# Kernel tuning notes

Hardware: AMD Instinct MI355X
Metric: run time of the kernel (lower is better)

## Reference

```python
import jax, jax.numpy as jnp
import numpy as np

WINDOW = 128
LOOK_BACKWARD = 1
LOOK_FORWARD = 0
DIM_HEAD = 64
ROPE_BASE = 10000.0


def look_around(x, backward=LOOK_BACKWARD, forward=LOOK_FORWARD, pad_value=-1):
    # x: [b, w, n, ...] -> pad window axis, gather shifted windows, concat along n axis
    w = x.shape[1]
    pads = [(0, 0)] * x.ndim
    pads[1] = (backward, forward)
    padded = jnp.pad(x, pads, constant_values=pad_value)
    return jnp.concatenate([padded[:, i:i + w] for i in range(backward + forward + 1)], axis=2)


def _rotate_half(x):
    x1, x2 = jnp.split(x, 2, axis=-1)
    return jnp.concatenate([-x2, x1], axis=-1)


def apply_rotary(bq, bk):
    # sinusoidal embeddings computed over the look-around key length j; queries use the last n positions
    j = bk.shape[2]
    n = bq.shape[2]
    inv_freq = 1.0 / (ROPE_BASE ** (jnp.arange(0, DIM_HEAD, 2, dtype=jnp.float32) / DIM_HEAD))
    t = jnp.arange(j, dtype=jnp.float32)
    freqs = t[:, None] * inv_freq[None, :]          # [j, d/2]
    freqs = jnp.concatenate([freqs, freqs], axis=-1)  # [j, d]
    q_freqs = freqs[-n:]
    bq = bq * jnp.cos(q_freqs) + _rotate_half(bq) * jnp.sin(q_freqs)
    bk = bk * jnp.cos(freqs) + _rotate_half(bk) * jnp.sin(freqs)
    return bq, bk


def setup_inputs() -> dict:
    key = jax.random.key(0)
    kq, kk, kv = jax.random.split(key, 3)
    shape = (4, 8, 4096, 64)
    return {
        'q': jax.random.normal(kq, shape, dtype=jnp.float32),
        'k': jax.random.normal(kk, shape, dtype=jnp.float32),
        'v': jax.random.normal(kv, shape, dtype=jnp.float32),
    }


def reference(q, k, v):
    B, H, N, D = q.shape
    b = B * H
    q_ = q.reshape(b, N, D)
    k_ = k.reshape(b, N, D)
    v_ = v.reshape(b, N, D)
    w = N // WINDOW
    scale = D ** -0.5

    seq = jnp.arange(N)
    b_t = seq.reshape(1, w, WINDOW)                           # [1, w, n]

    bq = q_.reshape(b, w, WINDOW, D) * scale
    bk = look_around(k_.reshape(b, w, WINDOW, D), pad_value=-1.0)  # [b, w, j, d]
    bv = look_around(v_.reshape(b, w, WINDOW, D), pad_value=-1.0)

    bq, bk = apply_rotary(bq, bk)

    bq_t = b_t[..., :, None]                                  # [1, w, n, 1]
    bq_k = look_around(b_t, pad_value=-1)[..., None, :]        # [1, w, 1, j]
    pad_mask = bq_k == -1
    causal_mask = bq_t < bq_k

    sim = jnp.einsum('bwie,bwje->bwij', bq, bk)                # [b, w, n, j]
    mask_value = -jnp.finfo(sim.dtype).max
    sim = jnp.where(causal_mask | pad_mask, mask_value, sim)

    attn = jax.nn.softmax(sim, axis=-1)
    out = jnp.einsum('bwij,bwje->bwie', attn, bv)
    return out.reshape(B, H, N, D)
```

## Files before the change

kernel.cpp:

```cpp
#include <hip/hip_runtime.h>
#include <float.h>

typedef __attribute__((ext_vector_type(8))) _Float16 f16x8;
typedef __attribute__((ext_vector_type(4))) _Float16 f16x4;
typedef __attribute__((ext_vector_type(4))) float f32x4;

#define WIN 128
#define SEQ 4096
#define DH 64
#define KSTR 72
#define VSTR 260
#define PC 40
#define VOFF 36864
#define POFF (VOFF + DH * VSTR * 2)
#define L2B_OVER 0.41524101186092156f

__launch_bounds__(512, 4)
__global__ void lattn_kernel(const float* __restrict__ q,
                             const float* __restrict__ k,
                             const float* __restrict__ v,
                             float* __restrict__ out) {
  __shared__ __align__(16) char smem[POFF + 8 * 16 * PC * 2];
  _Float16* ksm = (_Float16*)smem;
  _Float16* vsm = (_Float16*)(smem + VOFF);
  _Float16* psm = (_Float16*)(smem + POFF);

  const int bid  = blockIdx.x;
  const int lbid = (bid & 7) * 128 + (bid >> 3);
  const int bh   = lbid >> 5;
  const int win  = lbid & 31;
  const int tid  = threadIdx.x;
  const int wv   = tid >> 6;
  const int lane = tid & 63;
  const int c    = lane & 15;
  const int g    = lane >> 4;

  const long kbase = (long)win * WIN - WIN;
  const float* kb = k + (size_t)bh * SEQ * DH;
  const float* vb = v + (size_t)bh * SEQ * DH;


  float4 klo[4], khi[4];
  #pragma unroll
  for (int it = 0; it < 4; ++it) {
    int hi  = it * 8 + wv;
    int row = c + 16 * (hi >> 1);
    int p   = g + 4 * (hi & 1);
    long grow = kbase + row; grow = grow < 0 ? 0 : grow;
    const float4* src = (const float4*)(kb + grow * DH);
    klo[it] = src[p];
    khi[it] = src[p + 8];
  }

  float4 vr[2][4];
  #pragma unroll
  for (int it = 0; it < 2; ++it) {
    int kq = g + 4 * (it * 8 + wv);
    #pragma unroll
    for (int i = 0; i < 4; ++i) {
      long grow = kbase + 4 * kq + i; grow = grow < 0 ? 0 : grow;
      vr[it][i] = *(const float4*)(vb + grow * DH + 4 * c);
    }
  }

  const int qrow = 16 * wv + c;
  const float* qp = q + ((size_t)bh * SEQ + (size_t)win * WIN + qrow) * DH;
  const float4 x0 = *(const float4*)(qp + 8 * g);
  const float4 x1 = *(const float4*)(qp + 8 * g + 4);
  const float4 y0 = *(const float4*)(qp + 8 * g + 32);
  const float4 y1 = *(const float4*)(qp + 8 * g + 36);

  #pragma unroll
  for (int it = 0; it < 4; ++it) {
    int hi  = it * 8 + wv;
    int row = c + 16 * (hi >> 1);
    int p   = g + 4 * (hi & 1);
    float pos = (float)row;
    f16x4 rl, rh;
    #pragma unroll
    for (int j = 0; j < 4; ++j) {
      float sn, cs;
      __sincosf(pos * exp2f(-(float)(4 * p + j) * L2B_OVER), &sn, &cs);
      float x = ((const float*)&klo[it])[j];
      float y = ((const float*)&khi[it])[j];
      rl[j] = (_Float16)(x * cs - y * sn);
      rh[j] = (_Float16)(y * cs + x * sn);
    }
    *(f16x4*)(&ksm[row * KSTR + 4 * p])      = rl;
    *(f16x4*)(&ksm[row * KSTR + 4 * p + 32]) = rh;
  }

  #pragma unroll
  for (int it = 0; it < 2; ++it) {
    int kq = g + 4 * (it * 8 + wv);
    #pragma unroll
    for (int j = 0; j < 4; ++j) {
      f16x4 w;
      #pragma unroll
      for (int i = 0; i < 4; ++i) w[i] = (_Float16)(((const float*)&vr[it][i])[j]);
      *(f16x4*)(&vsm[(4 * c + j) * VSTR + 4 * kq]) = w;
    }
  }

  f16x8 qf0, qf1;
  {
    float pos = (float)(128 + qrow);
    #pragma unroll
    for (int j = 0; j < 4; ++j) {
      float sn, cs;
      __sincosf(pos * exp2f(-(float)(8 * g + j) * L2B_OVER), &sn, &cs);
      float xa = ((const float*)&x0)[j], ya = ((const float*)&y0)[j];
      qf0[j]     = (_Float16)((xa * cs - ya * sn) * 0.125f);
      qf1[j]     = (_Float16)((ya * cs + xa * sn) * 0.125f);
      __sincosf(pos * exp2f(-(float)(8 * g + 4 + j) * L2B_OVER), &sn, &cs);
      float xb = ((const float*)&x1)[j], yb = ((const float*)&y1)[j];
      qf0[4 + j] = (_Float16)((xb * cs - yb * sn) * 0.125f);
      qf1[4 + j] = (_Float16)((yb * cs + xb * sn) * 0.125f);
    }
  }

  __syncthreads();

  f32x4 acc[16];
  #pragma unroll
  for (int mt = 0; mt < 16; ++mt) acc[mt] = (f32x4){0.f, 0.f, 0.f, 0.f};

  #pragma unroll
  for (int mt = 0; mt < 16; ++mt) {
    f16x8 kf0 = *(const f16x8*)(&ksm[(16 * mt + c) * KSTR + 8 * g]);
    f16x8 kf1 = *(const f16x8*)(&ksm[(16 * mt + c) * KSTR + 32 + 8 * g]);
    acc[mt] = __builtin_amdgcn_mfma_f32_16x16x32_f16(kf0, qf0, acc[mt], 0, 0, 0);
    acc[mt] = __builtin_amdgcn_mfma_f32_16x16x32_f16(kf1, qf1, acc[mt], 0, 0, 0);
  }

  const int qi   = qrow;
  const int kmin = (win == 0) ? 128 : 0;
  float m = -FLT_MAX;
  #pragma unroll
  for (int mt = 0; mt < 16; ++mt) {
    #pragma unroll
    for (int r = 0; r < 4; ++r) {
      int j = 16 * mt + 4 * g + r;
      bool ok = (j <= qi + 128) && (j >= kmin);
      float s = ok ? acc[mt][r] : -FLT_MAX;
      acc[mt][r] = s;
      m = fmaxf(m, s);
    }
  }
  m = fmaxf(m, __shfl_xor(m, 16));
  m = fmaxf(m, __shfl_xor(m, 32));

  float sm = 0.f;
  #pragma unroll
  for (int mt = 0; mt < 16; ++mt) {
    #pragma unroll
    for (int r = 0; r < 4; ++r) {
      float p = __expf(acc[mt][r] - m);
      acc[mt][r] = p;
      sm += p;
    }
  }
  sm += __shfl_xor(sm, 16);
  sm += __shfl_xor(sm, 32);
  const float rinv = 1.0f / sm;

  f32x4 oacc[4];
  #pragma unroll
  for (int nt = 0; nt < 4; ++nt) oacc[nt] = (f32x4){0.f, 0.f, 0.f, 0.f};

  _Float16* pw = psm + wv * 16 * PC;

  #pragma unroll
  for (int ks = 0; ks < 8; ++ks) {
    #pragma unroll
    for (int t = 0; t < 2; ++t) {
      int mt = 2 * ks + t;
      f16x4 pv4;
      #pragma unroll
      for (int r = 0; r < 4; ++r) pv4[r] = (_Float16)(acc[mt][r] * rinv);
      *(f16x4*)(&pw[c * PC + 16 * t + 4 * g]) = pv4;
    }
    f16x8 pf = *(const f16x8*)(&pw[c * PC + 8 * g]);
    #pragma unroll
    for (int nt = 0; nt < 4; ++nt) {
      f16x8 vf = *(const f16x8*)(&vsm[(16 * nt + c) * VSTR + 32 * ks + 8 * g]);
      oacc[nt] = __builtin_amdgcn_mfma_f32_16x16x32_f16(vf, pf, oacc[nt], 0, 0, 0);
    }
  }

  float* ob = out + ((size_t)bh * SEQ + (size_t)win * WIN + qrow) * DH;
  #pragma unroll
  for (int nt = 0; nt < 4; ++nt) {
    float4 o4 = {oacc[nt][0], oacc[nt][1], oacc[nt][2], oacc[nt][3]};
    *(float4*)(ob + 16 * nt + 4 * g) = o4;
  }
}

extern "C" void kernel_launch(void* const* d_in, const int* in_sizes, int n_in,
                              void* d_out, int out_size, void* d_ws, size_t ws_size,
                              hipStream_t stream) {
  const float* q = (const float*)d_in[0];
  const float* k = (const float*)d_in[1];
  const float* v = (const float*)d_in[2];
  float* out = (float*)d_out;
  dim3 grid(32 * 32);
  lattn_kernel<<<grid, 512, 0, stream>>>(q, k, v, out);
}
```

Measured before the change: 53.10 us.

## Precompute RoPE sin/cos table and restage P through aliased shared memory

A small pre-kernel now fills a position-by-frequency cos/sin table in the workspace, so the attention kernel loads table entries instead of running exp2 and sincos per element. The P staging buffer now reuses the K shared-memory region after an added barrier, and each wave writes half of its P row block at once before four MFMA steps, instead of the previous write-then-read per 32-column step. Changing VSTR and the P stride shifts LDS bank layout and total shared usage. In exchange the change adds a second launch per call, extra global table reads, an extra block-wide barrier, and explicit waitcnt/sched barriers that may limit overlap.

```diff
diff --git a/kernel.cpp b/kernel.cpp
--- a/kernel.cpp
+++ b/kernel.cpp
@@ -9,21 +9,31 @@
 #define SEQ 4096
 #define DH 64
 #define KSTR 72
-#define VSTR 260
-#define PC 40
+#define VSTR 264
+#define PSTR 136
 #define VOFF 36864
-#define POFF (VOFF + DH * VSTR * 2)
 #define L2B_OVER 0.41524101186092156f
+
+__global__ void rope_tbl_kernel(float* __restrict__ t) {
+  int i = blockIdx.x * 256 + threadIdx.x;
+  int pos = i >> 5, f = i & 31;
+  float inv = exp2f(-(float)f * L2B_OVER);
+  float s, c;
+  sincosf((float)pos * inv, &s, &c);
+  t[2 * i]     = c;
+  t[2 * i + 1] = s;
+}
 
 __launch_bounds__(512, 4)
 __global__ void lattn_kernel(const float* __restrict__ q,
                              const float* __restrict__ k,
                              const float* __restrict__ v,
+                             const float* __restrict__ tbl,
                              float* __restrict__ out) {
-  __shared__ __align__(16) char smem[POFF + 8 * 16 * PC * 2];
+  __shared__ __align__(16) char smem[70656];
   _Float16* ksm = (_Float16*)smem;
+  _Float16* psm = (_Float16*)smem;
   _Float16* vsm = (_Float16*)(smem + VOFF);
-  _Float16* psm = (_Float16*)(smem + POFF);
 
   const int bid  = blockIdx.x;
   const int lbid = (bid & 7) * 128 + (bid >> 3);
@@ -75,12 +85,14 @@
     int hi  = it * 8 + wv;
     int row = c + 16 * (hi >> 1);
     int p   = g + 4 * (hi & 1);
-    float pos = (float)row;
+    const float4* tb = (const float4*)(tbl + 2 * (row * 32 + 4 * p));
+    float tt[8];
+    *(float4*)(tt)     = tb[0];
+    *(float4*)(tt + 4) = tb[1];
     f16x4 rl, rh;
     #pragma unroll
     for (int j = 0; j < 4; ++j) {
-      float sn, cs;
-      __sincosf(pos * exp2f(-(float)(4 * p + j) * L2B_OVER), &sn, &cs);
+      float cs = tt[2 * j], sn = tt[2 * j + 1];
       float x = ((const float*)&klo[it])[j];
       float y = ((const float*)&khi[it])[j];
       rl[j] = (_Float16)(x * cs - y * sn);
@@ -104,18 +116,22 @@
 
   f16x8 qf0, qf1;
   {
-    float pos = (float)(128 + qrow);
+    const float4* tb = (const float4*)(tbl + 2 * ((128 + qrow) * 32 + 8 * g));
+    float tt[16];
+    *(float4*)(tt)      = tb[0];
+    *(float4*)(tt + 4)  = tb[1];
+    *(float4*)(tt + 8)  = tb[2];
+    *(float4*)(tt + 12) = tb[3];
     #pragma unroll
     for (int j = 0; j < 4; ++j) {
-      float sn, cs;
-      __sincosf(pos * exp2f(-(float)(8 * g + j) * L2B_OVER), &sn, &cs);
+      float cs = tt[2 * j], sn = tt[2 * j + 1];
       float xa = ((const float*)&x0)[j], ya = ((const float*)&y0)[j];
       qf0[j]     = (_Float16)((xa * cs - ya * sn) * 0.125f);
       qf1[j]     = (_Float16)((ya * cs + xa * sn) * 0.125f);
-      __sincosf(pos * exp2f(-(float)(8 * g + 4 + j) * L2B_OVER), &sn, &cs);
+      float cs2 = tt[8 + 2 * j], sn2 = tt[9 + 2 * j];
       float xb = ((const float*)&x1)[j], yb = ((const float*)&y1)[j];
-      qf0[4 + j] = (_Float16)((xb * cs - yb * sn) * 0.125f);
-      qf1[4 + j] = (_Float16)((yb * cs + xb * sn) * 0.125f);
+      qf0[4 + j] = (_Float16)((xb * cs2 - yb * sn2) * 0.125f);
+      qf1[4 + j] = (_Float16)((yb * cs2 + xb * sn2) * 0.125f);
     }
   }
 
@@ -164,27 +180,39 @@
   sm += __shfl_xor(sm, 32);
   const float rinv = 1.0f / sm;
 
+  __syncthreads();
+
   f32x4 oacc[4];
   #pragma unroll
   for (int nt = 0; nt < 4; ++nt) oacc[nt] = (f32x4){0.f, 0.f, 0.f, 0.f};
 
-  _Float16* pw = psm + wv * 16 * PC;
-
-  #pragma unroll
-  for (int ks = 0; ks < 8; ++ks) {
-    #pragma unroll
-    for (int t = 0; t < 2; ++t) {
-      int mt = 2 * ks + t;
+  _Float16* pw = psm + wv * 16 * PSTR;
+
+  #pragma unroll
+  for (int h = 0; h < 2; ++h) {
+    if (h) {
+      asm volatile("s_waitcnt lgkmcnt(0)" ::: "memory");
+      __builtin_amdgcn_sched_barrier(0);
+    }
+    #pragma unroll
+    for (int mt8 = 0; mt8 < 8; ++mt8) {
+      int mt = 8 * h + mt8;
       f16x4 pv4;
       #pragma unroll
       for (int r = 0; r < 4; ++r) pv4[r] = (_Float16)(acc[mt][r] * rinv);
-      *(f16x4*)(&pw[c * PC + 16 * t + 4 * g]) = pv4;
-    }
-    f16x8 pf = *(const f16x8*)(&pw[c * PC + 8 * g]);
-    #pragma unroll
-    for (int nt = 0; nt < 4; ++nt) {
-      f16x8 vf = *(const f16x8*)(&vsm[(16 * nt + c) * VSTR + 32 * ks + 8 * g]);
-      oacc[nt] = __builtin_amdgcn_mfma_f32_16x16x32_f16(vf, pf, oacc[nt], 0, 0, 0);
+      *(f16x4*)(&pw[c * PSTR + 16 * mt8 + 4 * g]) = pv4;
+    }
+    asm volatile("s_waitcnt lgkmcnt(0)" ::: "memory");
+    __builtin_amdgcn_sched_barrier(0);
+
+    #pragma unroll
+    for (int ks = 0; ks < 4; ++ks) {
+      f16x8 pf = *(const f16x8*)(&pw[c * PSTR + 32 * ks + 8 * g]);
+      #pragma unroll
+      for (int nt = 0; nt < 4; ++nt) {
+        f16x8 vf = *(const f16x8*)(&vsm[(16 * nt + c) * VSTR + 128 * h + 32 * ks + 8 * g]);
+        oacc[nt] = __builtin_amdgcn_mfma_f32_16x16x32_f16(vf, pf, oacc[nt], 0, 0, 0);
+      }
     }
   }
 
@@ -203,6 +231,8 @@
   const float* k = (const float*)d_in[1];
   const float* v = (const float*)d_in[2];
   float* out = (float*)d_out;
-  dim3 grid(32 * 32);
-  lattn_kernel<<<grid, 512, 0, stream>>>(q, k, v, out);
+  float* tbl = (float*)d_ws;
+
+  rope_tbl_kernel<<<dim3(32), 256, 0, stream>>>(tbl);
+  lattn_kernel<<<dim3(32 * 32), 512, 0, stream>>>(q, k, v, tbl, out);
 }
```

After: 44.04 us. 1.21x faster.
